# Optimization experiments

Hardware: AMD Instinct MI355X
Metric: run time of the kernel (lower is better)

Reference implementation:

```python
import jax, jax.numpy as jnp
import numpy as np

DIM = 1024
NUM_HEADS = 16
HD = DIM // NUM_HEADS  # 64
ROPE_DIM = 64
ROPE_BASE = 10000.0


def setup_inputs() -> dict:
    key = jax.random.key(0)
    ks = jax.random.split(key, 5)
    B, N = 2, 2048
    s = 0.02
    return {
        "x": jax.random.normal(ks[0], (B, N, DIM), dtype=jnp.float32),
        "qkv_w": jax.random.normal(ks[1], (3 * DIM, DIM), dtype=jnp.float32) * s,
        "qkv_b": jax.random.normal(ks[2], (3 * DIM,), dtype=jnp.float32) * s,
        "proj_w": jax.random.normal(ks[3], (DIM, DIM), dtype=jnp.float32) * s,
        "proj_b": jax.random.normal(ks[4], (DIM,), dtype=jnp.float32) * s,
    }


def _apply_rope(t):
    # t: [B, H, N, D] with D even; interleaved (even, odd) pair rotation
    D = t.shape[-1]
    N = t.shape[2]
    pos = jnp.arange(N, dtype=t.dtype)
    inv = 1.0 / (ROPE_BASE ** (jnp.arange(0, D, 2, dtype=t.dtype) / D))
    freqs = pos[:, None] * inv[None, :]          # [N, D/2]
    cos = jnp.cos(freqs)[None, None]             # [1,1,N,D/2]
    sin = jnp.sin(freqs)[None, None]
    e = t[..., 0::2]
    o = t[..., 1::2]
    eo = e * cos - o * sin
    oo = e * sin + o * cos
    return jnp.stack([eo, oo], axis=-1).reshape(t.shape)


def reference(x, qkv_w, qkv_b, proj_w, proj_b):
    B, N, C = x.shape
    H, D = NUM_HEADS, HD
    scale = D ** -0.5
    qkv = x @ qkv_w.T + qkv_b                     # [B,N,3C]
    qkv = qkv.reshape(B, N, 3, H, D).transpose(2, 0, 3, 1, 4)  # [3,B,H,N,D]
    q, k, v = qkv[0], qkv[1], qkv[2]
    # RoPE on first ROPE_DIM dims of each head (here ROPE_DIM == HD)
    q = jnp.concatenate([_apply_rope(q[..., :ROPE_DIM]), q[..., ROPE_DIM:]], axis=-1)
    k = jnp.concatenate([_apply_rope(k[..., :ROPE_DIM]), k[..., ROPE_DIM:]], axis=-1)
    attn = jnp.einsum('bhnd,bhmd->bhnm', q, k) * scale
    attn = jax.nn.softmax(attn, axis=-1)
    out = jnp.einsum('bhnm,bhmd->bhnd', attn, v)  # [B,H,N,D]
    out = out.transpose(0, 2, 1, 3).reshape(B, N, C)
    return out @ proj_w.T + proj_b
```

## Files before the change

### kernel.cpp

```cpp
#include <hip/hip_runtime.h>
#include <hip/hip_bf16.h>
#include <stdint.h>

#define DIM   1024
#define NH    16
#define HDIM  64
#define SEQ   2048
#define BATCH 2
#define BHN   32
#define MTOK  4096
#define SC2   0.18033688f

using u16 = unsigned short;
using u32 = unsigned int;
typedef __attribute__((ext_vector_type(8))) short short8;
typedef __attribute__((ext_vector_type(4))) float f32x4;
typedef __attribute__((ext_vector_type(16))) float f32x16;

__device__ __forceinline__ u16 f2bf(float f) {
  __hip_bfloat16 h = __float2bfloat16(f);
  return *reinterpret_cast<u16*>(&h);
}
__device__ __forceinline__ u32 pk2(float lo, float hi) {
  return (u32)f2bf(lo) | ((u32)f2bf(hi) << 16);
}
__device__ __forceinline__ u32 cvtpk(float lo, float hi) {
  u32 r;
  asm("v_cvt_pk_bf16_f32 %0, %1, %2" : "=v"(r) : "v"(lo), "v"(hi));
  return r;
}
__device__ __forceinline__ float vexp2(float x) {
  float r;
  asm("v_exp_f32 %0, %1" : "=v"(r) : "v"(x));
  return r;
}

__device__ __forceinline__ void gload16(const void* g, void* lds) {
  __builtin_amdgcn_global_load_lds(
      (const __attribute__((address_space(1))) u32*)g,
      (__attribute__((address_space(3))) u32*)lds, 16, 0, 0);
}

#define PREP_A 1048576
#define PREP_B 1835008
#define PREP_C 2097152
#define PREP_E 2162688
__global__ void k_prep(const float4* __restrict__ x, const float4* __restrict__ qw,
                       const float4* __restrict__ pw, ushort4* __restrict__ xb,
                       ushort4* __restrict__ qwb, ushort4* __restrict__ pwb,
                       float2* __restrict__ tab) {
  int i = blockIdx.x * blockDim.x + threadIdx.x;
  if (i < PREP_A) {
    float4 v = x[i];
    xb[i] = make_ushort4(f2bf(v.x), f2bf(v.y), f2bf(v.z), f2bf(v.w));
  } else if (i < PREP_B) {
    int j = i - PREP_A;
    float4 v = qw[j];
    qwb[j] = make_ushort4(f2bf(v.x), f2bf(v.y), f2bf(v.z), f2bf(v.w));
  } else if (i < PREP_C) {
    int j = i - PREP_B;
    float4 v = pw[j];
    pwb[j] = make_ushort4(f2bf(v.x), f2bf(v.y), f2bf(v.z), f2bf(v.w));
  } else if (i < PREP_E) {
    int j = i - PREP_C;
    int n = j >> 5, f = j & 31;
    float inv = powf(10000.f, -(2.f * f) / 64.f);
    float s, c;
    sincosf((float)n * inv, &s, &c);
    tab[j] = make_float2(c, s);
  }
}

template <int EPI>
__global__ __launch_bounds__(256, 2) void k_gemm(
    const u16* __restrict__ A, const u16* __restrict__ Bt,
    const float* __restrict__ bias, int K,
    float* __restrict__ out_f, u16* __restrict__ qb, u16* __restrict__ kb,
    u16* __restrict__ vtb, const float2* __restrict__ tab) {
  __shared__ u16 As[128 * 64];
  __shared__ u16 Bs[128 * 64];
  const int tid = threadIdx.x;
  const int wid = tid >> 6, lane = tid & 63;
  const int lq = lane & 15, g = lane >> 4;
  const int wr = wid >> 1, wc = wid & 1;
  const int bid = blockIdx.x;
  const int xcd = bid & 7, idx = bid >> 3;
  const int brow = (xcd * 4 + (idx & 3)) * 128;
  const int bcol = (idx >> 2) * 128;
  f32x4 acc[4][4] = {};
  const u16* Ab = A + (size_t)brow * K;
  const u16* Bb = Bt + (size_t)bcol * K;

  for (int k0 = 0; k0 < K; k0 += 64) {
#pragma unroll
    for (int t = 0; t < 4; t++) {
      int rl = wid * 32 + t * 8 + (lane >> 3);
      int cs = (lane & 7) ^ (rl & 7);
      gload16(Ab + (size_t)rl * K + k0 + cs * 8, &As[(wid * 32 + t * 8) * 64]);
      gload16(Bb + (size_t)rl * K + k0 + cs * 8, &Bs[(wid * 32 + t * 8) * 64]);
    }
    __syncthreads();
#pragma unroll
    for (int kc = 0; kc < 2; kc++) {
      short8 af[4], bfr[4];
#pragma unroll
      for (int mt = 0; mt < 4; mt++) {
        int r = wr * 64 + mt * 16 + lq;
        af[mt] = *reinterpret_cast<const short8*>(&As[r * 64 + (((kc * 4 + g) ^ (r & 7)) * 8)]);
      }
#pragma unroll
      for (int nt = 0; nt < 4; nt++) {
        int r = wc * 64 + nt * 16 + lq;
        bfr[nt] = *reinterpret_cast<const short8*>(&Bs[r * 64 + (((kc * 4 + g) ^ (r & 7)) * 8)]);
      }
#pragma unroll
      for (int mt = 0; mt < 4; mt++)
#pragma unroll
        for (int nt = 0; nt < 4; nt++)
          acc[mt][nt] = __builtin_amdgcn_mfma_f32_16x16x32_bf16(af[mt], bfr[nt], acc[mt][nt], 0, 0, 0);
    }
    __syncthreads();
  }

#pragma unroll
  for (int mt = 0; mt < 4; mt++) {
    int row0 = brow + wr * 64 + mt * 16 + g * 4;
#pragma unroll
    for (int nt = 0; nt < 4; nt++) {
      int col = bcol + wc * 64 + nt * 16 + lq;
      float bv = bias[col];
      float v0 = acc[mt][nt][0] + bv;
      float v1 = acc[mt][nt][1] + bv;
      float v2 = acc[mt][nt][2] + bv;
      float v3 = acc[mt][nt][3] + bv;

      if (EPI == 1) {
        int which = col >> 10;
        if (which == 2) {
          int hd = col & 1023, d = hd & 63;
          int bb = row0 >> 11, n0 = row0 & 2047;
          int bh = bb * NH + (hd >> 6);
          uint2 pv = make_uint2(pk2(v0, v1), pk2(v2, v3));
          size_t idx2 = ((((size_t)bh * 32 + (n0 >> 6)) * 8 + ((n0 >> 3) & 7)) * 64 + d) * 8 + (n0 & 7);
          *reinterpret_cast<uint2*>(&vtb[idx2]) = pv;
          continue;
        }
      }

      { float u = (lane & 1) ? v0 : v1; float s = __shfl_xor(u, 1); if (lane & 1) v0 = s; else v1 = s; }
      { float u = (lane & 1) ? v2 : v3; float s = __shfl_xor(u, 1); if (lane & 1) v2 = s; else v3 = s; }
      { float u = (lane & 2) ? v0 : v2; float s = __shfl_xor(u, 2); if (lane & 2) v0 = s; else v2 = s; }
      { float u = (lane & 2) ? v1 : v3; float s = __shfl_xor(u, 2); if (lane & 2) v1 = s; else v3 = s; }
      const int rr = row0 + (lane & 3);
      const int f0 = col & ~3;

      if (EPI == 0) {
        *reinterpret_cast<float4*>(&out_f[(size_t)rr * DIM + f0]) = make_float4(v0, v1, v2, v3);
      } else {
        int which = f0 >> 10, hd = f0 & 1023, hdh = hd >> 6, d0 = hd & 63;
        int bb = rr >> 11, n = rr & 2047;
        int bh = bb * NH + hdh;
        float2 cs0 = tab[n * 32 + (d0 >> 1)];
        float2 cs1 = tab[n * 32 + (d0 >> 1) + 1];
        float e0 = fmaf(-v1, cs0.y, v0 * cs0.x);
        float o0 = fmaf( v0, cs0.y, v1 * cs0.x);
        float e1 = fmaf(-v3, cs1.y, v2 * cs1.x);
        float o1 = fmaf( v2, cs1.y, v3 * cs1.x);
        if (which == 0) {
          uint2 pv = make_uint2(pk2(e0 * SC2, o0 * SC2), pk2(e1 * SC2, o1 * SC2));
          *reinterpret_cast<uint2*>(&qb[((size_t)bh * SEQ + n) * HDIM + d0]) = pv;
        } else {
          size_t idx2 = ((((size_t)bh * 32 + (n >> 6)) * 8 + (d0 >> 3)) * 64 + (n & 63)) * 8 + (d0 & 7);
          *reinterpret_cast<uint2*>(&kb[idx2]) = make_uint2(pk2(e0, o0), pk2(e1, o1));
        }
      }
    }
  }
}

__global__ __launch_bounds__(256) void k_attn(
    const u16* __restrict__ qg, const u16* __restrict__ kg,
    const u16* __restrict__ vg, u16* __restrict__ aout) {
  __shared__ __align__(16) char smem[65536];
  const int tid = threadIdx.x;
  const int wid = tid >> 6, lane = tid & 63;
  const int l31 = lane & 31, h = lane >> 5;

  const int bid = blockIdx.x;
  const int xcd = bid & 7, slot = bid >> 3;
  const int bh = xcd * 4 + (slot >> 4);
  const int qt = slot & 15;
  const int b = bh >> 4, hh = bh & 15;
  const int q0 = qt * 128 + wid * 32;

  const u16* kbase = kg + (size_t)bh * SEQ * HDIM;
  const u16* vbase = vg + (size_t)bh * SEQ * HDIM;

  const u16* qrow = qg + ((size_t)bh * SEQ + q0 + l31) * HDIM;
  short8 qf[4];
#pragma unroll
  for (int c = 0; c < 4; c++)
    qf[c] = *reinterpret_cast<const short8*>(qrow + c * 16 + h * 8);

  short8 ones;
#pragma unroll
  for (int i = 0; i < 8; i++) ones[i] = (short)0x3F80;

  int koff[4];
#pragma unroll
  for (int c = 0; c < 4; c++)
    koff[c] = (2 * c + h) * 1024 + l31 * 16;

  f32x16 sA0, sA1, sB0, sB1;
  f32x16 oA = {}, oB = {}, ls = {};

  auto stage = [&](int buf, int tidx) {
    char* kd = smem + buf * 16384;
    const u16* kt = kbase + (size_t)tidx * 4096 + lane * 8;
    const u16* vt = vbase + (size_t)tidx * 4096 + lane * 8;
#pragma unroll
    for (int i = 0; i < 2; i++) {
      int g = wid + i * 4;
      gload16(kt + g * 512, kd + g * 1024);
      gload16(vt + g * 512, kd + 8192 + g * 1024);
    }
  };

  const int NT = SEQ / 64;

  auto body = [&](f32x16& sc0, f32x16& sc1, f32x16& sn0, f32x16& sn1, int t, bool last) {
    if (!last) asm volatile("s_waitcnt vmcnt(4)" ::: "memory");
    else       asm volatile("s_waitcnt vmcnt(0)" ::: "memory");
    __builtin_amdgcn_s_barrier();

    const char* kbp = smem + (t & 3) * 16384;
    const char* vbp = smem + ((t - 1) & 3) * 16384 + 8192;

#pragma unroll
    for (int c = 0; c < 4; c++) {
      short8 kf0 = *reinterpret_cast<const short8*>(kbp + koff[c]);
      short8 kf1 = *reinterpret_cast<const short8*>(kbp + koff[c] + 512);
      __builtin_amdgcn_s_setprio(1);
      if (c == 0) {
        f32x16 z = {};
        sn0 = __builtin_amdgcn_mfma_f32_32x32x16_bf16(kf0, qf[0], z, 0, 0, 0);
        sn1 = __builtin_amdgcn_mfma_f32_32x32x16_bf16(kf1, qf[0], z, 0, 0, 0);
      } else {
        sn0 = __builtin_amdgcn_mfma_f32_32x32x16_bf16(kf0, qf[c], sn0, 0, 0, 0);
        sn1 = __builtin_amdgcn_mfma_f32_32x32x16_bf16(kf1, qf[c], sn1, 0, 0, 0);
      }
      __builtin_amdgcn_s_setprio(0);

      if (c == 0 && t + 2 < NT) stage((t + 2) & 3, t + 2);

      short8 vf0 = *reinterpret_cast<const short8*>(vbp + koff[c]);
      short8 vf1 = *reinterpret_cast<const short8*>(vbp + koff[c] + 512);

      f32x16& sv = (c < 2) ? sc0 : sc1;
      const int e0 = (c & 1) * 8;
      float e[8];
#pragma unroll
      for (int j = 0; j < 8; j++) e[j] = vexp2(sv[e0 + j]);
      u32 a0 = cvtpk(e[0], e[1]), a1 = cvtpk(e[2], e[3]);
      u32 b0 = cvtpk(e[4], e[5]), b1 = cvtpk(e[6], e[7]);
      auto r0 = __builtin_amdgcn_permlane32_swap(a0, b0, false, false);
      auto r1 = __builtin_amdgcn_permlane32_swap(a1, b1, false, false);
      union { u32 u[4]; short8 v; } pp;
      pp.u[0] = r0[0]; pp.u[1] = r1[0]; pp.u[2] = r0[1]; pp.u[3] = r1[1];
      short8 pf = pp.v;

      __builtin_amdgcn_s_setprio(1);
      oA = __builtin_amdgcn_mfma_f32_32x32x16_bf16(vf0,  pf, oA, 0, 0, 0);
      oB = __builtin_amdgcn_mfma_f32_32x32x16_bf16(vf1,  pf, oB, 0, 0, 0);
      ls = __builtin_amdgcn_mfma_f32_32x32x16_bf16(ones, pf, ls, 0, 0, 0);
      __builtin_amdgcn_s_setprio(0);
    }
  };

  stage(0, 0);
  stage(1, 1);
  asm volatile("s_waitcnt vmcnt(4)" ::: "memory");
  __builtin_amdgcn_s_barrier();
  {
    const char* kbp = smem;
    f32x16 z = {};
    sA0 = z; sA1 = z;
#pragma unroll
    for (int c = 0; c < 4; c++) {
      short8 kf0 = *reinterpret_cast<const short8*>(kbp + koff[c]);
      short8 kf1 = *reinterpret_cast<const short8*>(kbp + koff[c] + 512);
      __builtin_amdgcn_s_setprio(1);
      sA0 = __builtin_amdgcn_mfma_f32_32x32x16_bf16(kf0, qf[c], sA0, 0, 0, 0);
      sA1 = __builtin_amdgcn_mfma_f32_32x32x16_bf16(kf1, qf[c], sA1, 0, 0, 0);
      __builtin_amdgcn_s_setprio(0);
      if (c == 0) stage(2, 2);
    }
  }

#pragma unroll 1
  for (int i = 0; i < 15; i++) {
    body(sA0, sA1, sB0, sB1, 2 * i + 1, false);
    body(sB0, sB1, sA0, sA1, 2 * i + 2, false);
  }
  body(sA0, sA1, sB0, sB1, 31, true);

  {
    const char* vbp = smem + 3 * 16384 + 8192;
#pragma unroll
    for (int c = 0; c < 4; c++) {
      short8 vf0 = *reinterpret_cast<const short8*>(vbp + koff[c]);
      short8 vf1 = *reinterpret_cast<const short8*>(vbp + koff[c] + 512);
      f32x16& sv = (c < 2) ? sB0 : sB1;
      const int e0 = (c & 1) * 8;
      float e[8];
#pragma unroll
      for (int j = 0; j < 8; j++) e[j] = vexp2(sv[e0 + j]);
      u32 a0 = cvtpk(e[0], e[1]), a1 = cvtpk(e[2], e[3]);
      u32 b0 = cvtpk(e[4], e[5]), b1 = cvtpk(e[6], e[7]);
      auto r0 = __builtin_amdgcn_permlane32_swap(a0, b0, false, false);
      auto r1 = __builtin_amdgcn_permlane32_swap(a1, b1, false, false);
      union { u32 u[4]; short8 v; } pp;
      pp.u[0] = r0[0]; pp.u[1] = r1[0]; pp.u[2] = r0[1]; pp.u[3] = r1[1];
      short8 pf = pp.v;
      oA = __builtin_amdgcn_mfma_f32_32x32x16_bf16(vf0,  pf, oA, 0, 0, 0);
      oB = __builtin_amdgcn_mfma_f32_32x32x16_bf16(vf1,  pf, oB, 0, 0, 0);
      ls = __builtin_amdgcn_mfma_f32_32x32x16_bf16(ones, pf, ls, 0, 0, 0);
    }
  }

  float invl = 1.0f / ls[0];
  int n = q0 + l31;
  u16* op = aout + ((size_t)(b * SEQ + n)) * DIM + hh * HDIM;
#pragma unroll
  for (int g = 0; g < 4; g++) {
    u32 w0 = pk2(oA[4 * g] * invl, oA[4 * g + 1] * invl);
    u32 w1 = pk2(oA[4 * g + 2] * invl, oA[4 * g + 3] * invl);
    *reinterpret_cast<uint2*>(op + 8 * g + 4 * h) = make_uint2(w0, w1);
    u32 x0 = pk2(oB[4 * g] * invl, oB[4 * g + 1] * invl);
    u32 x1 = pk2(oB[4 * g + 2] * invl, oB[4 * g + 3] * invl);
    *reinterpret_cast<uint2*>(op + 32 + 8 * g + 4 * h) = make_uint2(x0, x1);
  }
}

extern "C" void kernel_launch(void* const* d_in, const int* in_sizes, int n_in,
                              void* d_out, int out_size, void* d_ws, size_t ws_size,
                              hipStream_t stream) {
  (void)in_sizes; (void)n_in; (void)out_size; (void)ws_size;
  const float* x      = (const float*)d_in[0];
  const float* qkv_w  = (const float*)d_in[1];
  const float* qkv_b  = (const float*)d_in[2];
  const float* proj_w = (const float*)d_in[3];
  const float* proj_b = (const float*)d_in[4];
  float* out = (float*)d_out;

  char* w = (char*)d_ws;
  u16* xb     = (u16*)w;  w += (size_t)MTOK * DIM * 2;
  u16* wqkvb  = (u16*)w;  w += (size_t)3 * DIM * DIM * 2;
  u16* wprojb = (u16*)w;  w += (size_t)DIM * DIM * 2;
  u16* qb     = (u16*)w;  w += (size_t)BHN * SEQ * HDIM * 2;
  u16* kb     = (u16*)w;  w += (size_t)BHN * SEQ * HDIM * 2;
  u16* vtb    = (u16*)w;  w += (size_t)BHN * SEQ * HDIM * 2;
  u16* aout   = (u16*)w;  w += (size_t)MTOK * DIM * 2;
  float2* tab = (float2*)w;

  k_prep<<<(PREP_E + 255) / 256, 256, 0, stream>>>(
      (const float4*)x, (const float4*)qkv_w, (const float4*)proj_w,
      (ushort4*)xb, (ushort4*)wqkvb, (ushort4*)wprojb, tab);

  k_gemm<1><<<768, 256, 0, stream>>>(
      xb, wqkvb, qkv_b, DIM, nullptr, qb, kb, vtb, tab);

  k_attn<<<512, 256, 0, stream>>>(qb, kb, vtb, aout);

  k_gemm<0><<<256, 256, 0, stream>>>(
      aout, wprojb, proj_b, DIM, out, nullptr, nullptr, nullptr, nullptr);
}
```

Before: 111.8 us.

## Load V tiles directly from global into registers, keep only K in LDS

```diff
diff --git a/kernel.cpp b/kernel.cpp
--- a/kernel.cpp
+++ b/kernel.cpp
@@ -181,7 +181,7 @@
 __global__ __launch_bounds__(256) void k_attn(
     const u16* __restrict__ qg, const u16* __restrict__ kg,
     const u16* __restrict__ vg, u16* __restrict__ aout) {
-  __shared__ __align__(16) char smem[65536];
+  __shared__ __align__(16) char smem[32768];
   const int tid = threadIdx.x;
   const int wid = tid >> 6, lane = tid & 63;
   const int l31 = lane & 31, h = lane >> 5;
@@ -194,7 +194,7 @@
   const int q0 = qt * 128 + wid * 32;
 
   const u16* kbase = kg + (size_t)bh * SEQ * HDIM;
-  const u16* vbase = vg + (size_t)bh * SEQ * HDIM;
+  const u16* vb0   = vg + (size_t)bh * SEQ * HDIM + h * 512 + l31 * 8;
 
   const u16* qrow = qg + ((size_t)bh * SEQ + q0 + l31) * HDIM;
   short8 qf[4];
@@ -213,28 +213,33 @@
 
   f32x16 sA0, sA1, sB0, sB1;
   f32x16 oA = {}, oB = {}, ls = {};
-
-  auto stage = [&](int buf, int tidx) {
-    char* kd = smem + buf * 16384;
+  short8 vfA[8], vfB[8];
+
+  auto stageK = [&](int buf, int tidx) {
+    char* kd = smem + buf * 8192;
     const u16* kt = kbase + (size_t)tidx * 4096 + lane * 8;
-    const u16* vt = vbase + (size_t)tidx * 4096 + lane * 8;
-#pragma unroll
-    for (int i = 0; i < 2; i++) {
-      int g = wid + i * 4;
-      gload16(kt + g * 512, kd + g * 1024);
-      gload16(vt + g * 512, kd + 8192 + g * 1024);
-    }
+    gload16(kt + wid * 512,       kd + wid * 1024);
+    gload16(kt + (wid + 4) * 512, kd + (wid + 4) * 1024);
   };
 
   const int NT = SEQ / 64;
 
-  auto body = [&](f32x16& sc0, f32x16& sc1, f32x16& sn0, f32x16& sn1, int t, bool last) {
-    if (!last) asm volatile("s_waitcnt vmcnt(4)" ::: "memory");
+  auto body = [&](f32x16& sc0, f32x16& sc1, f32x16& sn0, f32x16& sn1,
+                  short8 (&vc)[8], short8 (&vn)[8], int t, bool last) {
+    if (!last) asm volatile("s_waitcnt vmcnt(2)" ::: "memory");
     else       asm volatile("s_waitcnt vmcnt(0)" ::: "memory");
     __builtin_amdgcn_s_barrier();
 
-    const char* kbp = smem + (t & 3) * 16384;
-    const char* vbp = smem + ((t - 1) & 3) * 16384 + 8192;
+    const char* kbp = smem + (t & 3) * 8192;
+
+    {
+      const u16* vn_p = vb0 + (size_t)t * 4096;
+#pragma unroll
+      for (int c = 0; c < 4; c++) {
+        vn[2 * c]     = *reinterpret_cast<const short8*>(vn_p + c * 1024);
+        vn[2 * c + 1] = *reinterpret_cast<const short8*>(vn_p + c * 1024 + 256);
+      }
+    }
 
 #pragma unroll
     for (int c = 0; c < 4; c++) {
@@ -251,10 +256,7 @@
       }
       __builtin_amdgcn_s_setprio(0);
 
-      if (c == 0 && t + 2 < NT) stage((t + 2) & 3, t + 2);
-
-      short8 vf0 = *reinterpret_cast<const short8*>(vbp + koff[c]);
-      short8 vf1 = *reinterpret_cast<const short8*>(vbp + koff[c] + 512);
+      if (c == 0 && t + 2 < NT) stageK((t + 2) & 3, t + 2);
 
       f32x16& sv = (c < 2) ? sc0 : sc1;
       const int e0 = (c & 1) * 8;
@@ -270,18 +272,23 @@
       short8 pf = pp.v;
 
       __builtin_amdgcn_s_setprio(1);
-      oA = __builtin_amdgcn_mfma_f32_32x32x16_bf16(vf0,  pf, oA, 0, 0, 0);
-      oB = __builtin_amdgcn_mfma_f32_32x32x16_bf16(vf1,  pf, oB, 0, 0, 0);
-      ls = __builtin_amdgcn_mfma_f32_32x32x16_bf16(ones, pf, ls, 0, 0, 0);
+      oA = __builtin_amdgcn_mfma_f32_32x32x16_bf16(vc[2 * c],     pf, oA, 0, 0, 0);
+      oB = __builtin_amdgcn_mfma_f32_32x32x16_bf16(vc[2 * c + 1], pf, oB, 0, 0, 0);
+      ls = __builtin_amdgcn_mfma_f32_32x32x16_bf16(ones,          pf, ls, 0, 0, 0);
       __builtin_amdgcn_s_setprio(0);
     }
   };
 
-  stage(0, 0);
-  stage(1, 1);
-  asm volatile("s_waitcnt vmcnt(4)" ::: "memory");
+  stageK(0, 0);
+  stageK(1, 1);
+  asm volatile("s_waitcnt vmcnt(2)" ::: "memory");
   __builtin_amdgcn_s_barrier();
   {
+#pragma unroll
+    for (int c = 0; c < 4; c++) {
+      vfA[2 * c]     = *reinterpret_cast<const short8*>(vb0 + c * 1024);
+      vfA[2 * c + 1] = *reinterpret_cast<const short8*>(vb0 + c * 1024 + 256);
+    }
     const char* kbp = smem;
     f32x16 z = {};
     sA0 = z; sA1 = z;
@@ -293,39 +300,34 @@
       sA0 = __builtin_amdgcn_mfma_f32_32x32x16_bf16(kf0, qf[c], sA0, 0, 0, 0);
       sA1 = __builtin_amdgcn_mfma_f32_32x32x16_bf16(kf1, qf[c], sA1, 0, 0, 0);
       __builtin_amdgcn_s_setprio(0);
-      if (c == 0) stage(2, 2);
+      if (c == 0) stageK(2, 2);
     }
   }
 
 #pragma unroll 1
   for (int i = 0; i < 15; i++) {
-    body(sA0, sA1, sB0, sB1, 2 * i + 1, false);
-    body(sB0, sB1, sA0, sA1, 2 * i + 2, false);
-  }
-  body(sA0, sA1, sB0, sB1, 31, true);
-
-  {
-    const char* vbp = smem + 3 * 16384 + 8192;
-#pragma unroll
-    for (int c = 0; c < 4; c++) {
-      short8 vf0 = *reinterpret_cast<const short8*>(vbp + koff[c]);
-      short8 vf1 = *reinterpret_cast<const short8*>(vbp + koff[c] + 512);
-      f32x16& sv = (c < 2) ? sB0 : sB1;
-      const int e0 = (c & 1) * 8;
-      float e[8];
-#pragma unroll
-      for (int j = 0; j < 8; j++) e[j] = vexp2(sv[e0 + j]);
-      u32 a0 = cvtpk(e[0], e[1]), a1 = cvtpk(e[2], e[3]);
-      u32 b0 = cvtpk(e[4], e[5]), b1 = cvtpk(e[6], e[7]);
-      auto r0 = __builtin_amdgcn_permlane32_swap(a0, b0, false, false);
-      auto r1 = __builtin_amdgcn_permlane32_swap(a1, b1, false, false);
-      union { u32 u[4]; short8 v; } pp;
-      pp.u[0] = r0[0]; pp.u[1] = r1[0]; pp.u[2] = r0[1]; pp.u[3] = r1[1];
-      short8 pf = pp.v;
-      oA = __builtin_amdgcn_mfma_f32_32x32x16_bf16(vf0,  pf, oA, 0, 0, 0);
-      oB = __builtin_amdgcn_mfma_f32_32x32x16_bf16(vf1,  pf, oB, 0, 0, 0);
-      ls = __builtin_amdgcn_mfma_f32_32x32x16_bf16(ones, pf, ls, 0, 0, 0);
-    }
+    body(sA0, sA1, sB0, sB1, vfA, vfB, 2 * i + 1, false);
+    body(sB0, sB1, sA0, sA1, vfB, vfA, 2 * i + 2, false);
+  }
+  body(sA0, sA1, sB0, sB1, vfA, vfB, 31, true);
+
+#pragma unroll
+  for (int c = 0; c < 4; c++) {
+    f32x16& sv = (c < 2) ? sB0 : sB1;
+    const int e0 = (c & 1) * 8;
+    float e[8];
+#pragma unroll
+    for (int j = 0; j < 8; j++) e[j] = vexp2(sv[e0 + j]);
+    u32 a0 = cvtpk(e[0], e[1]), a1 = cvtpk(e[2], e[3]);
+    u32 b0 = cvtpk(e[4], e[5]), b1 = cvtpk(e[6], e[7]);
+    auto r0 = __builtin_amdgcn_permlane32_swap(a0, b0, false, false);
+    auto r1 = __builtin_amdgcn_permlane32_swap(a1, b1, false, false);
+    union { u32 u[4]; short8 v; } pp;
+    pp.u[0] = r0[0]; pp.u[1] = r1[0]; pp.u[2] = r0[1]; pp.u[3] = r1[1];
+    short8 pf = pp.v;
+    oA = __builtin_amdgcn_mfma_f32_32x32x16_bf16(vfB[2 * c],     pf, oA, 0, 0, 0);
+    oB = __builtin_amdgcn_mfma_f32_32x32x16_bf16(vfB[2 * c + 1], pf, oB, 0, 0, 0);
+    ls = __builtin_amdgcn_mfma_f32_32x32x16_bf16(ones,           pf, ls, 0, 0, 0);
   }
 
   float invl = 1.0f / ls[0];
```

After: 114.6 us. 1.03x slower.
